# Kernel optimization log

Hardware: AMD Instinct MI355X
Metric: run time of the kernel (lower is better)

The kernel has to match this reference:

```python
import jax, jax.numpy as jnp
import numpy as np

# Constants from mode='only_tv': gamma_l1=gamma_dwt=beta=lambda_l1=lambda_dwt=sigma=0,
# so u_l1,u_dwt,z,eta_l1,eta_dwt,rho stay identically zero and drop out of the math.
GAMMA_TV = 2.0
ALPHA = 5.0
LAMBDA_TV = 1e-4
N_ITER = 200


def soft_thresh(v, t):
    return jnp.sign(v) * jnp.maximum(jnp.abs(v) - t, 0.0)


def setup_inputs() -> dict:
    key = jax.random.key(0)
    k1, k2, k3 = jax.random.split(key, 3)
    target = jax.random.normal(k1, (4096, 64), dtype=jnp.float32)  # B spectra of K bands
    A = jax.random.normal(k2, (9, 64), dtype=jnp.float32) * 0.1     # (M=9 channels, K=64 bands)
    x0 = jax.random.normal(k3, (4096, 64), dtype=jnp.float32)       # replaces randn_like(target)
    return {"target": target, "A": A, "x0": x0}


def reference(target, A, x0):
    # target, x0: (B, K) batch of per-sample length-K vectors; A: (M, K)
    K = A.shape[1]
    AT = A.T  # (K, M)
    I = jnp.eye(K, dtype=A.dtype)
    Delta = jnp.roll(I, 1, axis=1) - I          # (K, K)
    DtD = Delta.T @ Delta
    inv_item = jnp.linalg.inv(AT @ A + GAMMA_TV * DtD + ALPHA * I)  # (K, K)

    # b = A @ x  per sample  ->  (B, M);  AT @ b per sample -> (B, K)
    b = target @ A.T
    ATb = b @ A

    # per-sample Delta @ v, batched over rows -> v_mat @ Delta.T
    def D(v):
        return v @ Delta.T

    eta_tv0 = jnp.zeros_like(x0)
    tau0 = jnp.zeros_like(x0)

    def step(carry, _):
        x, eta_tv, tau = carry
        u_tv = soft_thresh(D(x) + eta_tv / GAMMA_TV, LAMBDA_TV / GAMMA_TV)
        w = jnp.maximum(x + tau / ALPHA, 0.0)
        # note: torch's matmul(z_tv, DeltaT) on a vector equals Delta @ z_tv -> batched D(.)
        resid = ATb + D(GAMMA_TV * u_tv - eta_tv) + ALPHA * w - tau
        x = resid @ inv_item.T  # per-sample inv_item @ resid
        eta_tv = eta_tv + GAMMA_TV * (D(x) - u_tv)
        tau = tau + ALPHA * (x - w)
        return (x, eta_tv, tau), None

    (x, _, _), _ = jax.lax.scan(step, (x0, eta_tv0, tau0), None, length=N_ITER)
    return x
```

## Files before the change

### kernel.cpp

```cpp
#include <hip/hip_runtime.h>

#define NSAMP 4096
#define NITER 200

__global__ __launch_bounds__(256) void setup_woodbury(const float* __restrict__ A,
                                                      float* __restrict__ mperm) {
  __shared__ double lamr[64];
  __shared__ float binv[64];
  __shared__ float P[9][64];
  __shared__ float Q[9][64];
  __shared__ double W[9][18];
  __shared__ float Mfull[64][64];
  const int tid = threadIdx.x;
  const double TWO_PI = 6.283185307179586476925286766559;

  double cb = 0.0;
  if (tid < 64) {
    cb = cos(TWO_PI * (double)tid / 64.0);
    lamr[tid] = 1.0 / (9.0 - 4.0 * cb);
  }
  __syncthreads();
  if (tid < 64) {
    double cm1 = 1.0, c0 = cb;
    double acc = lamr[0] + cb * lamr[1];
#pragma unroll 16
    for (int m = 2; m < 64; ++m) {
      double c = 2.0 * cb * c0 - cm1;
      cm1 = c0;
      c0 = c;
      acc += c * lamr[m];
    }
    binv[tid] = (float)(acc / 64.0);
  }
  __syncthreads();

  for (int e = tid; e < 9 * 64; e += 256) {
    int m = e >> 6, i = e & 63;
    double acc = 0.0;
#pragma unroll 16
    for (int k = 0; k < 64; ++k)
      acc += (double)A[m * 64 + k] * (double)binv[(k - i) & 63];
    P[m][i] = (float)acc;
  }
  __syncthreads();

  if (tid < 81) {
    int m = tid / 9, n = tid % 9;
    double acc = (m == n) ? 1.0 : 0.0;
#pragma unroll 16
    for (int i = 0; i < 64; ++i)
      acc += (double)P[m][i] * (double)A[n * 64 + i];
    W[m][n] = acc;
    W[m][n + 9] = (m == n) ? 1.0 : 0.0;
  }
  __syncthreads();

  {
    const int r9 = tid / 18, c9 = tid % 18;
    const bool act = (tid < 162);
    for (int k = 0; k < 9; ++k) {
      double pv = 1.0, f = 0.0, wkc = 0.0;
      if (act) {
        pv = W[k][k];
        f = W[r9][k];
        wkc = W[k][c9];
      }
      __syncthreads();
      if (act) {
        double nk = wkc / pv;
        W[r9][c9] = (r9 == k) ? nk : fma(-f, nk, W[r9][c9]);
      }
      __syncthreads();
    }
  }

  for (int e = tid; e < 9 * 64; e += 256) {
    int m = e >> 6, j = e & 63;
    double acc = 0.0;
#pragma unroll
    for (int n = 0; n < 9; ++n) acc += W[m][n + 9] * (double)P[n][j];
    Q[m][j] = (float)acc;
  }
  __syncthreads();

  for (int e = tid; e < 64 * 64; e += 256) {
    int i = e >> 6, j = e & 63;
    float acc = binv[(i - j) & 63];
#pragma unroll
    for (int m = 0; m < 9; ++m) acc = fmaf(-P[m][i], Q[m][j], acc);
    Mfull[i][j] = acc;
  }
  __syncthreads();

  if (tid < 64) {
    const int lid = tid;
    int dpp1;
    asm volatile(
        "s_nop 4\n\t"
        "v_mov_b32_dpp %0, %1 row_ror:1 row_mask:0xf bank_mask:0xf\n\t"
        "s_nop 4"
        : "=v"(dpp1)
        : "v"(lid));
    const int lane0val = __builtin_amdgcn_readfirstlane(dpp1);
    const int dir = (lane0val == 1) ? 1 : -1;
    const int xs4[4] = {0, 16, 48, 32};
    for (int s = 0; s < 4; ++s) {
      for (int t = 0; t < 16; ++t) {
        int q = (lid & 48) | (((lid & 15) + dir * t + 16) & 15);
        int j = q ^ xs4[s];
        mperm[lid * 64 + 16 * s + t] = Mfull[lid][j];
      }
    }
  }
}

#define DPL(op, acc, rr, mm, rot) \
  op " " acc ", " rr ", " mm " row_ror:" #rot " row_mask:0xf bank_mask:0xf\n\t"

__global__ __launch_bounds__(256)
void admm_kernel(const float* __restrict__ target, const float* __restrict__ A,
                 const float* __restrict__ x0, const float* __restrict__ mperm,
                 float* __restrict__ out) {
  const int tid = threadIdx.x;
  const int wid = tid >> 6;
  const int lane = tid & 63;
  const int s = blockIdx.x * 4 + wid;

  float t = target[s * 64 + lane];
  float atbv = 0.f;
#pragma unroll
  for (int m = 0; m < 9; ++m) {
    float a = A[m * 64 + lane];
    float p = t * a;
#pragma unroll
    for (int off = 32; off; off >>= 1) p += __shfl_xor(p, off, 64);
    atbv = fmaf(a, p, atbv);
  }

  const float* mrow = mperm + (size_t)lane * 64;
  unsigned int a_nxt = ((lane + 1) & 63) * 4;
  unsigned int a_x32 = (lane ^ 32) * 4;
  float xin = x0[s * 64 + lane];
  float xout;
  int cnt_s;
  const int smask = 0x7fffffff;
  const float sthr = 5e-5f, sc02 = 0.2f, sc5 = 5.0f;

  asm volatile(
      "s_mov_b32 m0, -1\n\t"
      "global_load_dwordx4 v[64:67],   %[mp], off\n\t"
      "global_load_dwordx4 v[68:71],   %[mp], off offset:16\n\t"
      "global_load_dwordx4 v[72:75],   %[mp], off offset:32\n\t"
      "global_load_dwordx4 v[76:79],   %[mp], off offset:48\n\t"
      "global_load_dwordx4 v[80:83],   %[mp], off offset:64\n\t"
      "global_load_dwordx4 v[84:87],   %[mp], off offset:80\n\t"
      "global_load_dwordx4 v[88:91],   %[mp], off offset:96\n\t"
      "global_load_dwordx4 v[92:95],   %[mp], off offset:112\n\t"
      "global_load_dwordx4 v[96:99],   %[mp], off offset:128\n\t"
      "global_load_dwordx4 v[100:103], %[mp], off offset:144\n\t"
      "global_load_dwordx4 v[104:107], %[mp], off offset:160\n\t"
      "global_load_dwordx4 v[108:111], %[mp], off offset:176\n\t"
      "global_load_dwordx4 v[112:115], %[mp], off offset:192\n\t"
      "global_load_dwordx4 v[116:119], %[mp], off offset:208\n\t"
      "global_load_dwordx4 v[120:123], %[mp], off offset:224\n\t"
      "global_load_dwordx4 v[124:127], %[mp], off offset:240\n\t"
      "v_mov_b32 v32, %[xin]\n\t"
      "v_mov_b32 v36, %[atb]\n\t"
      "v_mov_b32 v33, 0\n\t"
      "v_mov_b32 v34, 0\n\t"
      "ds_bpermute_b32 v45, %[anx], v32\n\t"
      "s_waitcnt lgkmcnt(0)\n\t"
      "v_sub_f32 v35, v45, v32\n\t"
      "s_movk_i32 %[cnt], 200\n\t"
      "s_waitcnt vmcnt(0)\n\t"
      "1:\n\t"
      "v_fma_f32 v40, 0.5, v33, v35\n\t"
      "v_and_b32 v41, %[msk], v40\n\t"
      "v_subrev_f32 v41, %[thr], v41\n\t"
      "v_max_f32 v41, 0, v41\n\t"
      "v_bfi_b32 v42, %[msk], v41, v40\n\t"
      "v_fma_f32 v43, %[c02], v34, v32\n\t"
      "v_max_f32 v43, 0, v43\n\t"
      "v_fma_f32 v40, 2.0, v42, -v33\n\t"
      "ds_bpermute_b32 v45, %[anx], v40\n\t"
      "v_fma_f32 v44, %[c5], v43, v36\n\t"
      "v_sub_f32 v44, v44, v34\n\t"
      "v_sub_f32 v44, v44, v40\n\t"
      "s_waitcnt lgkmcnt(0)\n\t"
      "v_add_f32 v44, v44, v45\n\t"
      "ds_swizzle_b32 v47, v44 offset:0x401F\n\t"
      "v_mul_f32 v37, v44, v64\n\t"
      DPL("v_mul_f32",  "v38", "v44", "v65", 1)
      DPL("v_mul_f32",  "v39", "v44", "v66", 2)
      DPL("v_mul_f32",  "v46", "v44", "v67", 3)
      DPL("v_fmac_f32", "v37", "v44", "v68", 4)
      DPL("v_fmac_f32", "v38", "v44", "v69", 5)
      DPL("v_fmac_f32", "v39", "v44", "v70", 6)
      DPL("v_fmac_f32", "v46", "v44", "v71", 7)
      DPL("v_fmac_f32", "v37", "v44", "v72", 8)
      DPL("v_fmac_f32", "v38", "v44", "v73", 9)
      DPL("v_fmac_f32", "v39", "v44", "v74", 10)
      DPL("v_fmac_f32", "v46", "v44", "v75", 11)
      DPL("v_fmac_f32", "v37", "v44", "v76", 12)
      DPL("v_fmac_f32", "v38", "v44", "v77", 13)
      DPL("v_fmac_f32", "v39", "v44", "v78", 14)
      DPL("v_fmac_f32", "v46", "v44", "v79", 15)
      "s_waitcnt lgkmcnt(0)\n\t"
      "ds_bpermute_b32 v48, %[a32], v47\n\t"
      "s_nop 1\n\t"
      "v_fmac_f32 v37, v47, v80\n\t"
      DPL("v_fmac_f32", "v38", "v47", "v81", 1)
      DPL("v_fmac_f32", "v39", "v47", "v82", 2)
      DPL("v_fmac_f32", "v46", "v47", "v83", 3)
      DPL("v_fmac_f32", "v37", "v47", "v84", 4)
      DPL("v_fmac_f32", "v38", "v47", "v85", 5)
      DPL("v_fmac_f32", "v39", "v47", "v86", 6)
      DPL("v_fmac_f32", "v46", "v47", "v87", 7)
      DPL("v_fmac_f32", "v37", "v47", "v88", 8)
      DPL("v_fmac_f32", "v38", "v47", "v89", 9)
      DPL("v_fmac_f32", "v39", "v47", "v90", 10)
      DPL("v_fmac_f32", "v46", "v47", "v91", 11)
      DPL("v_fmac_f32", "v37", "v47", "v92", 12)
      DPL("v_fmac_f32", "v38", "v47", "v93", 13)
      DPL("v_fmac_f32", "v39", "v47", "v94", 14)
      DPL("v_fmac_f32", "v46", "v47", "v95", 15)
      "s_waitcnt lgkmcnt(0)\n\t"
      "ds_swizzle_b32 v49, v48 offset:0x401F\n\t"
      "s_nop 1\n\t"
      "v_fmac_f32 v37, v48, v96\n\t"
      DPL("v_fmac_f32", "v38", "v48", "v97", 1)
      DPL("v_fmac_f32", "v39", "v48", "v98", 2)
      DPL("v_fmac_f32", "v46", "v48", "v99", 3)
      DPL("v_fmac_f32", "v37", "v48", "v100", 4)
      DPL("v_fmac_f32", "v38", "v48", "v101", 5)
      DPL("v_fmac_f32", "v39", "v48", "v102", 6)
      DPL("v_fmac_f32", "v46", "v48", "v103", 7)
      DPL("v_fmac_f32", "v37", "v48", "v104", 8)
      DPL("v_fmac_f32", "v38", "v48", "v105", 9)
      DPL("v_fmac_f32", "v39", "v48", "v106", 10)
      DPL("v_fmac_f32", "v46", "v48", "v107", 11)
      DPL("v_fmac_f32", "v37", "v48", "v108", 12)
      DPL("v_fmac_f32", "v38", "v48", "v109", 13)
      DPL("v_fmac_f32", "v39", "v48", "v110", 14)
      DPL("v_fmac_f32", "v46", "v48", "v111", 15)
      "s_waitcnt lgkmcnt(0)\n\t"
      "s_nop 1\n\t"
      "v_fmac_f32 v37, v49, v112\n\t"
      DPL("v_fmac_f32", "v38", "v49", "v113", 1)
      DPL("v_fmac_f32", "v39", "v49", "v114", 2)
      DPL("v_fmac_f32", "v46", "v49", "v115", 3)
      DPL("v_fmac_f32", "v37", "v49", "v116", 4)
      DPL("v_fmac_f32", "v38", "v49", "v117", 5)
      DPL("v_fmac_f32", "v39", "v49", "v118", 6)
      DPL("v_fmac_f32", "v46", "v49", "v119", 7)
      DPL("v_fmac_f32", "v37", "v49", "v120", 8)
      DPL("v_fmac_f32", "v38", "v49", "v121", 9)
      DPL("v_fmac_f32", "v39", "v49", "v122", 10)
      DPL("v_fmac_f32", "v46", "v49", "v123", 11)
      DPL("v_fmac_f32", "v37", "v49", "v124", 12)
      DPL("v_fmac_f32", "v38", "v49", "v125", 13)
      DPL("v_fmac_f32", "v39", "v49", "v126", 14)
      DPL("v_fmac_f32", "v46", "v49", "v127", 15)
      "v_add_f32 v37, v37, v38\n\t"
      "v_add_f32 v39, v39, v46\n\t"
      "v_add_f32 v32, v37, v39\n\t"
      "ds_bpermute_b32 v45, %[anx], v32\n\t"
      "v_sub_f32 v41, v32, v43\n\t"
      "v_fma_f32 v34, %[c5], v41, v34\n\t"
      "s_waitcnt lgkmcnt(0)\n\t"
      "v_sub_f32 v35, v45, v32\n\t"
      "v_sub_f32 v41, v35, v42\n\t"
      "v_fma_f32 v33, 2.0, v41, v33\n\t"
      "s_sub_u32 %[cnt], %[cnt], 1\n\t"
      "s_cmp_lg_u32 %[cnt], 0\n\t"
      "s_cbranch_scc1 1b\n\t"
      "v_mov_b32 %[xout], v32\n\t"
      : [xout] "=v"(xout), [cnt] "=&s"(cnt_s)
      : [mp] "v"(mrow), [anx] "v"(a_nxt), [a32] "v"(a_x32),
        [xin] "v"(xin), [atb] "v"(atbv),
        [msk] "s"(smask), [thr] "s"(sthr), [c02] "s"(sc02), [c5] "s"(sc5)
      : "memory", "scc",
        "v32","v33","v34","v35","v36","v37","v38","v39","v40","v41","v42","v43",
        "v44","v45","v46","v47","v48","v49","v64","v65","v66","v67",
        "v68","v69","v70","v71","v72","v73","v74","v75","v76","v77","v78","v79",
        "v80","v81","v82","v83","v84","v85","v86","v87","v88","v89","v90","v91",
        "v92","v93","v94","v95","v96","v97","v98","v99","v100","v101","v102",
        "v103","v104","v105","v106","v107","v108","v109","v110","v111","v112",
        "v113","v114","v115","v116","v117","v118","v119","v120","v121","v122",
        "v123","v124","v125","v126","v127");

  out[s * 64 + lane] = xout;
}

extern "C" void kernel_launch(void* const* d_in, const int* in_sizes, int n_in,
                              void* d_out, int out_size, void* d_ws, size_t ws_size,
                              hipStream_t stream) {
  const float* target = (const float*)d_in[0];
  const float* A = (const float*)d_in[1];
  const float* x0 = (const float*)d_in[2];
  float* out = (float*)d_out;
  float* mperm = (float*)d_ws;

  setup_woodbury<<<1, 256, 0, stream>>>(A, mperm);
  admm_kernel<<<NSAMP / 4, 256, 0, stream>>>(target, A, x0, mperm, out);
}
```

Before: 201.1 us.

## Fuse Woodbury setup into ADMM kernel and use LDS for matvec operands

Drops the single-block setup kernel and recomputes the 64x64 inverse in every block, building the permuted matrix in shared memory. The matrix rows are then loaded with ds_read instead of global loads. In the inner loop, the upper half of the per-iteration matvec now writes the residual vector to LDS and reads 32 contiguous values back, replacing the chained bpermute and swizzle cross-lane steps. This removes a kernel launch and serial dependency but repeats the setup work in each of 1024 blocks and uses about 40KB of LDS per block, which may limit occupancy.

```diff
diff --git a/kernel.cpp b/kernel.cpp
--- a/kernel.cpp
+++ b/kernel.cpp
@@ -3,15 +3,26 @@
 #define NSAMP 4096
 #define NITER 200
 
-__global__ __launch_bounds__(256) void setup_woodbury(const float* __restrict__ A,
-                                                      float* __restrict__ mperm) {
-  __shared__ double lamr[64];
-  __shared__ float binv[64];
-  __shared__ float P[9][64];
-  __shared__ float Q[9][64];
-  __shared__ double W[9][18];
-  __shared__ float Mfull[64][64];
+#define DPL(op, acc, rr, mm, rot) \
+  op " " acc ", " rr ", " mm " row_ror:" #rot " row_mask:0xf bank_mask:0xf\n\t"
+
+__global__ __launch_bounds__(256)
+void admm_fused(const float* __restrict__ target, const float* __restrict__ A,
+                const float* __restrict__ x0, float* __restrict__ out) {
+  __shared__ __align__(16) char smem[39952];
+  float (*Mfull)[64] = (float(*)[64])(smem);
+  float* Mperm       = (float*)(smem + 16384);
+  float (*rbuf)[64]  = (float(*)[64])(smem + 32768);
+  double* lamr       = (double*)(smem + 32768);
+  float* binv        = (float*)(smem + 33792);
+  float (*P)[64]     = (float(*)[64])(smem + 34048);
+  float (*Q)[64]     = (float(*)[64])(smem + 36352);
+  double (*W)[18]    = (double(*)[18])(smem + 38656);
+
   const int tid = threadIdx.x;
+  const int wid = tid >> 6;
+  const int lane = tid & 63;
+  const int s = blockIdx.x * 4 + wid;
   const double TWO_PI = 6.283185307179586476925286766559;
 
   double cb = 0.0;
@@ -92,39 +103,28 @@
   }
   __syncthreads();
 
-  if (tid < 64) {
-    const int lid = tid;
-    int dpp1;
-    asm volatile(
-        "s_nop 4\n\t"
-        "v_mov_b32_dpp %0, %1 row_ror:1 row_mask:0xf bank_mask:0xf\n\t"
-        "s_nop 4"
-        : "=v"(dpp1)
-        : "v"(lid));
-    const int lane0val = __builtin_amdgcn_readfirstlane(dpp1);
-    const int dir = (lane0val == 1) ? 1 : -1;
-    const int xs4[4] = {0, 16, 48, 32};
-    for (int s = 0; s < 4; ++s) {
-      for (int t = 0; t < 16; ++t) {
-        int q = (lid & 48) | (((lid & 15) + dir * t + 16) & 15);
-        int j = q ^ xs4[s];
-        mperm[lid * 64 + 16 * s + t] = Mfull[lid][j];
-      }
+  int dpp1;
+  asm volatile(
+      "s_nop 4\n\t"
+      "v_mov_b32_dpp %0, %1 row_ror:1 row_mask:0xf bank_mask:0xf\n\t"
+      "s_nop 4"
+      : "=v"(dpp1)
+      : "v"(lane));
+  const int dir = (__builtin_amdgcn_readfirstlane(dpp1) == 1) ? 1 : -1;
+
+  for (int e = tid; e < 64 * 64; e += 256) {
+    int li = e >> 6, k = e & 63;
+    int j;
+    if (k < 32) {
+      int t = k & 15;
+      int q = (li & 48) | (((li & 15) + dir * t + 16) & 15);
+      j = (k < 16) ? q : (q ^ 16);
+    } else {
+      j = ((li & 32) ^ 32) + (k - 32);
     }
-  }
-}
-
-#define DPL(op, acc, rr, mm, rot) \
-  op " " acc ", " rr ", " mm " row_ror:" #rot " row_mask:0xf bank_mask:0xf\n\t"
-
-__global__ __launch_bounds__(256)
-void admm_kernel(const float* __restrict__ target, const float* __restrict__ A,
-                 const float* __restrict__ x0, const float* __restrict__ mperm,
-                 float* __restrict__ out) {
-  const int tid = threadIdx.x;
-  const int wid = tid >> 6;
-  const int lane = tid & 63;
-  const int s = blockIdx.x * 4 + wid;
+    Mperm[li * 64 + k] = Mfull[li][j];
+  }
+  __syncthreads();
 
   float t = target[s * 64 + lane];
   float atbv = 0.f;
@@ -137,9 +137,11 @@
     atbv = fmaf(a, p, atbv);
   }
 
-  const float* mrow = mperm + (size_t)lane * 64;
+  unsigned int mprm = (unsigned int)(uintptr_t)(Mperm + lane * 64);
+  unsigned int rb = (unsigned int)(uintptr_t)(&rbuf[wid][0]);
+  unsigned int a_w = rb + lane * 4;
+  unsigned int a_rf = rb + (((lane & 32) ^ 32) << 2);
   unsigned int a_nxt = ((lane + 1) & 63) * 4;
-  unsigned int a_x32 = (lane ^ 32) * 4;
   float xin = x0[s * 64 + lane];
   float xout;
   int cnt_s;
@@ -148,22 +150,22 @@
 
   asm volatile(
       "s_mov_b32 m0, -1\n\t"
-      "global_load_dwordx4 v[64:67],   %[mp], off\n\t"
-      "global_load_dwordx4 v[68:71],   %[mp], off offset:16\n\t"
-      "global_load_dwordx4 v[72:75],   %[mp], off offset:32\n\t"
-      "global_load_dwordx4 v[76:79],   %[mp], off offset:48\n\t"
-      "global_load_dwordx4 v[80:83],   %[mp], off offset:64\n\t"
-      "global_load_dwordx4 v[84:87],   %[mp], off offset:80\n\t"
-      "global_load_dwordx4 v[88:91],   %[mp], off offset:96\n\t"
-      "global_load_dwordx4 v[92:95],   %[mp], off offset:112\n\t"
-      "global_load_dwordx4 v[96:99],   %[mp], off offset:128\n\t"
-      "global_load_dwordx4 v[100:103], %[mp], off offset:144\n\t"
-      "global_load_dwordx4 v[104:107], %[mp], off offset:160\n\t"
-      "global_load_dwordx4 v[108:111], %[mp], off offset:176\n\t"
-      "global_load_dwordx4 v[112:115], %[mp], off offset:192\n\t"
-      "global_load_dwordx4 v[116:119], %[mp], off offset:208\n\t"
-      "global_load_dwordx4 v[120:123], %[mp], off offset:224\n\t"
-      "global_load_dwordx4 v[124:127], %[mp], off offset:240\n\t"
+      "ds_read_b128 v[64:67],   %[mprm]\n\t"
+      "ds_read_b128 v[68:71],   %[mprm] offset:16\n\t"
+      "ds_read_b128 v[72:75],   %[mprm] offset:32\n\t"
+      "ds_read_b128 v[76:79],   %[mprm] offset:48\n\t"
+      "ds_read_b128 v[80:83],   %[mprm] offset:64\n\t"
+      "ds_read_b128 v[84:87],   %[mprm] offset:80\n\t"
+      "ds_read_b128 v[88:91],   %[mprm] offset:96\n\t"
+      "ds_read_b128 v[92:95],   %[mprm] offset:112\n\t"
+      "ds_read_b128 v[96:99],   %[mprm] offset:128\n\t"
+      "ds_read_b128 v[100:103], %[mprm] offset:144\n\t"
+      "ds_read_b128 v[104:107], %[mprm] offset:160\n\t"
+      "ds_read_b128 v[108:111], %[mprm] offset:176\n\t"
+      "ds_read_b128 v[112:115], %[mprm] offset:192\n\t"
+      "ds_read_b128 v[116:119], %[mprm] offset:208\n\t"
+      "ds_read_b128 v[120:123], %[mprm] offset:224\n\t"
+      "ds_read_b128 v[124:127], %[mprm] offset:240\n\t"
       "v_mov_b32 v32, %[xin]\n\t"
       "v_mov_b32 v36, %[atb]\n\t"
       "v_mov_b32 v33, 0\n\t"
@@ -172,7 +174,6 @@
       "s_waitcnt lgkmcnt(0)\n\t"
       "v_sub_f32 v35, v45, v32\n\t"
       "s_movk_i32 %[cnt], 200\n\t"
-      "s_waitcnt vmcnt(0)\n\t"
       "1:\n\t"
       "v_fma_f32 v40, 0.5, v33, v35\n\t"
       "v_and_b32 v41, %[msk], v40\n\t"
@@ -188,81 +189,86 @@
       "v_sub_f32 v44, v44, v40\n\t"
       "s_waitcnt lgkmcnt(0)\n\t"
       "v_add_f32 v44, v44, v45\n\t"
+      "ds_write_b32 %[aw], v44\n\t"
       "ds_swizzle_b32 v47, v44 offset:0x401F\n\t"
+      "ds_read_b128 v[48:51], %[arf]\n\t"
+      "ds_read_b128 v[52:55], %[arf] offset:16\n\t"
+      "ds_read_b128 v[56:59], %[arf] offset:32\n\t"
+      "ds_read_b128 v[60:63], %[arf] offset:48\n\t"
+      "ds_read_b128 v[16:19], %[arf] offset:64\n\t"
+      "ds_read_b128 v[20:23], %[arf] offset:80\n\t"
+      "ds_read_b128 v[24:27], %[arf] offset:96\n\t"
+      "ds_read_b128 v[28:31], %[arf] offset:112\n\t"
       "v_mul_f32 v37, v44, v64\n\t"
       DPL("v_mul_f32",  "v38", "v44", "v65", 1)
       DPL("v_mul_f32",  "v39", "v44", "v66", 2)
-      DPL("v_mul_f32",  "v46", "v44", "v67", 3)
+      DPL("v_mul_f32",  "v40", "v44", "v67", 3)
       DPL("v_fmac_f32", "v37", "v44", "v68", 4)
       DPL("v_fmac_f32", "v38", "v44", "v69", 5)
       DPL("v_fmac_f32", "v39", "v44", "v70", 6)
-      DPL("v_fmac_f32", "v46", "v44", "v71", 7)
+      DPL("v_fmac_f32", "v40", "v44", "v71", 7)
       DPL("v_fmac_f32", "v37", "v44", "v72", 8)
       DPL("v_fmac_f32", "v38", "v44", "v73", 9)
       DPL("v_fmac_f32", "v39", "v44", "v74", 10)
-      DPL("v_fmac_f32", "v46", "v44", "v75", 11)
+      DPL("v_fmac_f32", "v40", "v44", "v75", 11)
       DPL("v_fmac_f32", "v37", "v44", "v76", 12)
       DPL("v_fmac_f32", "v38", "v44", "v77", 13)
       DPL("v_fmac_f32", "v39", "v44", "v78", 14)
-      DPL("v_fmac_f32", "v46", "v44", "v79", 15)
-      "s_waitcnt lgkmcnt(0)\n\t"
-      "ds_bpermute_b32 v48, %[a32], v47\n\t"
+      DPL("v_fmac_f32", "v40", "v44", "v79", 15)
+      "s_waitcnt lgkmcnt(8)\n\t"
       "s_nop 1\n\t"
       "v_fmac_f32 v37, v47, v80\n\t"
       DPL("v_fmac_f32", "v38", "v47", "v81", 1)
       DPL("v_fmac_f32", "v39", "v47", "v82", 2)
-      DPL("v_fmac_f32", "v46", "v47", "v83", 3)
+      DPL("v_fmac_f32", "v40", "v47", "v83", 3)
       DPL("v_fmac_f32", "v37", "v47", "v84", 4)
       DPL("v_fmac_f32", "v38", "v47", "v85", 5)
       DPL("v_fmac_f32", "v39", "v47", "v86", 6)
-      DPL("v_fmac_f32", "v46", "v47", "v87", 7)
+      DPL("v_fmac_f32", "v40", "v47", "v87", 7)
       DPL("v_fmac_f32", "v37", "v47", "v88", 8)
       DPL("v_fmac_f32", "v38", "v47", "v89", 9)
       DPL("v_fmac_f32", "v39", "v47", "v90", 10)
-      DPL("v_fmac_f32", "v46", "v47", "v91", 11)
+      DPL("v_fmac_f32", "v40", "v47", "v91", 11)
       DPL("v_fmac_f32", "v37", "v47", "v92", 12)
       DPL("v_fmac_f32", "v38", "v47", "v93", 13)
       DPL("v_fmac_f32", "v39", "v47", "v94", 14)
-      DPL("v_fmac_f32", "v46", "v47", "v95", 15)
+      DPL("v_fmac_f32", "v40", "v47", "v95", 15)
+      "s_waitcnt lgkmcnt(4)\n\t"
+      "v_fmac_f32 v37, v48, v96\n\t"
+      "v_fmac_f32 v38, v49, v97\n\t"
+      "v_fmac_f32 v39, v50, v98\n\t"
+      "v_fmac_f32 v40, v51, v99\n\t"
+      "v_fmac_f32 v37, v52, v100\n\t"
+      "v_fmac_f32 v38, v53, v101\n\t"
+      "v_fmac_f32 v39, v54, v102\n\t"
+      "v_fmac_f32 v40, v55, v103\n\t"
+      "v_fmac_f32 v37, v56, v104\n\t"
+      "v_fmac_f32 v38, v57, v105\n\t"
+      "v_fmac_f32 v39, v58, v106\n\t"
+      "v_fmac_f32 v40, v59, v107\n\t"
+      "v_fmac_f32 v37, v60, v108\n\t"
+      "v_fmac_f32 v38, v61, v109\n\t"
+      "v_fmac_f32 v39, v62, v110\n\t"
+      "v_fmac_f32 v40, v63, v111\n\t"
       "s_waitcnt lgkmcnt(0)\n\t"
-      "ds_swizzle_b32 v49, v48 offset:0x401F\n\t"
-      "s_nop 1\n\t"
-      "v_fmac_f32 v37, v48, v96\n\t"
-      DPL("v_fmac_f32", "v38", "v48", "v97", 1)
-      DPL("v_fmac_f32", "v39", "v48", "v98", 2)
-      DPL("v_fmac_f32", "v46", "v48", "v99", 3)
-      DPL("v_fmac_f32", "v37", "v48", "v100", 4)
-      DPL("v_fmac_f32", "v38", "v48", "v101", 5)
-      DPL("v_fmac_f32", "v39", "v48", "v102", 6)
-      DPL("v_fmac_f32", "v46", "v48", "v103", 7)
-      DPL("v_fmac_f32", "v37", "v48", "v104", 8)
-      DPL("v_fmac_f32", "v38", "v48", "v105", 9)
-      DPL("v_fmac_f32", "v39", "v48", "v106", 10)
-      DPL("v_fmac_f32", "v46", "v48", "v107", 11)
-      DPL("v_fmac_f32", "v37", "v48", "v108", 12)
-      DPL("v_fmac_f32", "v38", "v48", "v109", 13)
-      DPL("v_fmac_f32", "v39", "v48", "v110", 14)
-      DPL("v_fmac_f32", "v46", "v48", "v111", 15)
-      "s_waitcnt lgkmcnt(0)\n\t"
-      "s_nop 1\n\t"
-      "v_fmac_f32 v37, v49, v112\n\t"
-      DPL("v_fmac_f32", "v38", "v49", "v113", 1)
-      DPL("v_fmac_f32", "v39", "v49", "v114", 2)
-      DPL("v_fmac_f32", "v46", "v49", "v115", 3)
-      DPL("v_fmac_f32", "v37", "v49", "v116", 4)
-      DPL("v_fmac_f32", "v38", "v49", "v117", 5)
-      DPL("v_fmac_f32", "v39", "v49", "v118", 6)
-      DPL("v_fmac_f32", "v46", "v49", "v119", 7)
-      DPL("v_fmac_f32", "v37", "v49", "v120", 8)
-      DPL("v_fmac_f32", "v38", "v49", "v121", 9)
-      DPL("v_fmac_f32", "v39", "v49", "v122", 10)
-      DPL("v_fmac_f32", "v46", "v49", "v123", 11)
-      DPL("v_fmac_f32", "v37", "v49", "v124", 12)
-      DPL("v_fmac_f32", "v38", "v49", "v125", 13)
-      DPL("v_fmac_f32", "v39", "v49", "v126", 14)
-      DPL("v_fmac_f32", "v46", "v49", "v127", 15)
+      "v_fmac_f32 v37, v16, v112\n\t"
+      "v_fmac_f32 v38, v17, v113\n\t"
+      "v_fmac_f32 v39, v18, v114\n\t"
+      "v_fmac_f32 v40, v19, v115\n\t"
+      "v_fmac_f32 v37, v20, v116\n\t"
+      "v_fmac_f32 v38, v21, v117\n\t"
+      "v_fmac_f32 v39, v22, v118\n\t"
+      "v_fmac_f32 v40, v23, v119\n\t"
+      "v_fmac_f32 v37, v24, v120\n\t"
+      "v_fmac_f32 v38, v25, v121\n\t"
+      "v_fmac_f32 v39, v26, v122\n\t"
+      "v_fmac_f32 v40, v27, v123\n\t"
+      "v_fmac_f32 v37, v28, v124\n\t"
+      "v_fmac_f32 v38, v29, v125\n\t"
+      "v_fmac_f32 v39, v30, v126\n\t"
+      "v_fmac_f32 v40, v31, v127\n\t"
       "v_add_f32 v37, v37, v38\n\t"
-      "v_add_f32 v39, v39, v46\n\t"
+      "v_add_f32 v39, v39, v40\n\t"
       "v_add_f32 v32, v37, v39\n\t"
       "ds_bpermute_b32 v45, %[anx], v32\n\t"
       "v_sub_f32 v41, v32, v43\n\t"
@@ -276,12 +282,15 @@
       "s_cbranch_scc1 1b\n\t"
       "v_mov_b32 %[xout], v32\n\t"
       : [xout] "=v"(xout), [cnt] "=&s"(cnt_s)
-      : [mp] "v"(mrow), [anx] "v"(a_nxt), [a32] "v"(a_x32),
+      : [mprm] "v"(mprm), [aw] "v"(a_w), [arf] "v"(a_rf), [anx] "v"(a_nxt),
         [xin] "v"(xin), [atb] "v"(atbv),
         [msk] "s"(smask), [thr] "s"(sthr), [c02] "s"(sc02), [c5] "s"(sc5)
       : "memory", "scc",
+        "v16","v17","v18","v19","v20","v21","v22","v23","v24","v25","v26","v27",
+        "v28","v29","v30","v31",
         "v32","v33","v34","v35","v36","v37","v38","v39","v40","v41","v42","v43",
-        "v44","v45","v46","v47","v48","v49","v64","v65","v66","v67",
+        "v44","v45","v46","v47","v48","v49","v50","v51","v52","v53","v54","v55",
+        "v56","v57","v58","v59","v60","v61","v62","v63","v64","v65","v66","v67",
         "v68","v69","v70","v71","v72","v73","v74","v75","v76","v77","v78","v79",
         "v80","v81","v82","v83","v84","v85","v86","v87","v88","v89","v90","v91",
         "v92","v93","v94","v95","v96","v97","v98","v99","v100","v101","v102",
@@ -299,8 +308,6 @@
   const float* A = (const float*)d_in[1];
   const float* x0 = (const float*)d_in[2];
   float* out = (float*)d_out;
-  float* mperm = (float*)d_ws;
-
-  setup_woodbury<<<1, 256, 0, stream>>>(A, mperm);
-  admm_kernel<<<NSAMP / 4, 256, 0, stream>>>(target, A, x0, mperm, out);
+
+  admm_fused<<<NSAMP / 4, 256, 0, stream>>>(target, A, x0, out);
 }
```

Result: faster. 187.4 us (-6.8%).
